# Optimization experiments

Measured on AMD Instinct MI355X. Metric: run time of the kernel, lower is better.

The kernel has to match this reference:

```python
import jax, jax.numpy as jnp
import numpy as np

D = 1024      # model_dimension
H = 16        # num_heads
HD = D // H   # head_dimension (shared K/V head dim)
B, S = 2, 2048


def setup_inputs() -> dict:
    key = jax.random.key(0)
    ks = jax.random.split(key, 11)
    s = 0.02
    return {
        "q": jax.random.normal(ks[0], (B, S, D), jnp.float32),
        "k": jax.random.normal(ks[1], (B, S, D), jnp.float32),
        "v": jax.random.normal(ks[2], (B, S, D), jnp.float32),
        "Wq": jax.random.normal(ks[3], (D, D), jnp.float32) * s,
        "bq": jnp.zeros((D,), jnp.float32),
        "Wk": jax.random.normal(ks[4], (D, HD), jnp.float32) * s,
        "bk": jnp.zeros((HD,), jnp.float32),
        "Wv": jax.random.normal(ks[5], (D, HD), jnp.float32) * s,
        "bv": jnp.zeros((HD,), jnp.float32),
        "Wo": jax.random.normal(ks[6], (D, D), jnp.float32) * s,
        "bo": jnp.zeros((D,), jnp.float32),
    }


def reference(q, k, v, Wq, bq, Wk, bk, Wv, bv, Wo, bo):
    Bsz, Sq, Dm = q.shape
    # Q projection + split into heads: (B, H, Sq, HD)
    qh = (q @ Wq + bq).reshape(Bsz, Sq, H, HD).transpose(0, 2, 1, 3)
    # Shared single K/V head: (B, Sk, HD)
    kh = k @ Wk + bk
    vh = v @ Wv + bv
    # Scores (B, H, Sq, Sk), scaled then clamped as in the original
    scores = jnp.einsum('bhqd,bkd->bhqk', qh, kh) / jnp.sqrt(jnp.float32(HD))
    scores = jnp.clip(scores, -1e6, 1e6)
    attn = jax.nn.softmax(scores, axis=-1)
    out = jnp.einsum('bhqk,bkd->bhqd', attn, vh)
    out = out.transpose(0, 2, 1, 3).reshape(Bsz, Sq, Dm)
    return out @ Wo + bo
```

## Files before the change

kernel.cpp:

```cpp
#include <hip/hip_runtime.h>
#include <cstdint>
#include <cstddef>

typedef unsigned short u16;
typedef uint32_t u32;
typedef __bf16 bf16x8 __attribute__((ext_vector_type(8)));
typedef float  f32x4  __attribute__((ext_vector_type(4)));
typedef u16    u16x4  __attribute__((ext_vector_type(4)));

#define DEV static __device__ __forceinline__
#define MFMA16(a, b, c) __builtin_amdgcn_mfma_f32_16x16x32_bf16(a, b, c, 0, 0, 0)

DEV u16 f2bf(float x) {
  unsigned u = __float_as_uint(x);
  u += 0x7fffu + ((u >> 16) & 1u);
  return (u16)(u >> 16);
}

DEV u32 cvt_pk_bf16(float lo, float hi) {
  u32 r;
  asm("v_cvt_pk_bf16_f32 %0, %1, %2" : "=v"(r) : "v"(lo), "v"(hi));
  return r;
}

DEV void gload_lds16(const void* g, void* l) {
  __builtin_amdgcn_global_load_lds(
      (__attribute__((address_space(1))) void*)(void*)g,
      (__attribute__((address_space(3))) void*)l, 16, 0, 0);
}

__global__ void k_convert3(const float* __restrict__ a, const float* __restrict__ b,
                           const float* __restrict__ c, u16* __restrict__ oa,
                           u16* __restrict__ ob, u16* __restrict__ oc, int n4) {
  int i = blockIdx.x * blockDim.x + threadIdx.x;
  if (i >= n4) return;
  const float* src = blockIdx.y == 0 ? a : blockIdx.y == 1 ? b : c;
  u16* dst = blockIdx.y == 0 ? oa : blockIdx.y == 1 ? ob : oc;
  f32x4 f = reinterpret_cast<const f32x4*>(src)[i];
  u16x4 o;
  o[0] = f2bf(f[0]); o[1] = f2bf(f[1]); o[2] = f2bf(f[2]); o[3] = f2bf(f[3]);
  reinterpret_cast<u16x4*>(dst)[i] = o;
}

__global__ void k_transpose2(const float* __restrict__ in0, u16* __restrict__ out0,
                             const float* __restrict__ in1, u16* __restrict__ out1,
                             int R, int C) {
  __shared__ float tile[32][33];
  const float* in = blockIdx.z ? in1 : in0;
  u16* out = blockIdx.z ? out1 : out0;
  int bx = blockIdx.x * 32, by = blockIdx.y * 32;
  int tx = threadIdx.x, ty = threadIdx.y;
#pragma unroll
  for (int j = 0; j < 4; ++j)
    tile[ty + j * 8][tx] = in[(size_t)(by + ty + j * 8) * C + bx + tx];
  __syncthreads();
#pragma unroll
  for (int j = 0; j < 4; ++j)
    out[(size_t)(bx + ty + j * 8) * R + by + tx] = f2bf(tile[tx][ty + j * 8]);
}

template <bool OUT_BF16>
__global__ __launch_bounds__(512) void k_gemm128(const u16* __restrict__ A, const u16* __restrict__ Bt,
                                                 const float* __restrict__ bias, void* __restrict__ Cout,
                                                 int M, int N, int K, float scale) {
  __shared__ u16 As[128 * 32];
  __shared__ u16 Bs[128 * 32];
  const int tid = threadIdx.x, lane = tid & 63, wid = tid >> 6;
  const int s = blockIdx.x;
  const int xr = s & 7, t = s >> 3;
  const int bx = t & 7;
  const int by = (t >> 3) * 8 + xr;
  const int brow = by * 128, bcol = bx * 128;
  const int wr = (wid >> 2) * 64, wc = (wid & 3) * 32;

  const int e0 = wid * 512 + lane * 8;
  const u16* a0 = A + (size_t)(brow + (e0 >> 5)) * K + (e0 & 31);
  const u16* b0 = Bt + (size_t)(bcol + (e0 >> 5)) * K + (e0 & 31);
  u16* lA = As + wid * 512;
  u16* lB = Bs + wid * 512;

  f32x4 acc[4][2] = {};
  for (int k0 = 0; k0 < K; k0 += 32) {
    gload_lds16(a0 + k0, lA);
    gload_lds16(b0 + k0, lB);
    __syncthreads();
    const int lr = lane & 15, lk = (lane >> 4) * 8;
    bf16x8 af[4], bfr[2];
#pragma unroll
    for (int m = 0; m < 4; ++m) af[m] = *(const bf16x8*)&As[(wr + m * 16 + lr) * 32 + lk];
#pragma unroll
    for (int n = 0; n < 2; ++n) bfr[n] = *(const bf16x8*)&Bs[(wc + n * 16 + lr) * 32 + lk];
#pragma unroll
    for (int m = 0; m < 4; ++m)
#pragma unroll
      for (int n = 0; n < 2; ++n) acc[m][n] = MFMA16(af[m], bfr[n], acc[m][n]);
    __syncthreads();
  }

  const int lr = lane & 15, lg = lane >> 4;
#pragma unroll
  for (int m = 0; m < 4; ++m)
#pragma unroll
    for (int n = 0; n < 2; ++n) {
      const int col = bcol + wc + n * 16 + lr;
      const float bv = bias ? bias[col] : 0.f;
#pragma unroll
      for (int r = 0; r < 4; ++r) {
        const int row = brow + wr + m * 16 + lg * 4 + r;
        float val = (acc[m][n][r] + bv) * scale;
        if constexpr (OUT_BF16) ((u16*)Cout)[(size_t)row * N + col] = f2bf(val);
        else ((float*)Cout)[(size_t)row * N + col] = val;
      }
    }
}

__global__ __launch_bounds__(256) void k_gemm64(const u16* __restrict__ A0, const u16* __restrict__ A1,
                                                const u16* __restrict__ Bt0, const u16* __restrict__ Bt1,
                                                const float* __restrict__ bias0, const float* __restrict__ bias1,
                                                u16* __restrict__ C0, u16* __restrict__ C1, int K) {
  __shared__ u16 As[64 * 32];
  __shared__ u16 Bs[64 * 32];
  const int sel = blockIdx.y;
  const u16* A = sel ? A1 : A0;
  const u16* Bt = sel ? Bt1 : Bt0;
  const float* bias = sel ? bias1 : bias0;
  const int tid = threadIdx.x, lane = tid & 63, wid = tid >> 6;
  const int brow = blockIdx.x * 64;
  const int e0 = wid * 512 + lane * 8;
  const u16* a0 = A + (size_t)(brow + (e0 >> 5)) * K + (e0 & 31);
  const u16* b0 = Bt + (size_t)(e0 >> 5) * K + (e0 & 31);
  u16* lA = As + wid * 512;
  u16* lB = Bs + wid * 512;
  f32x4 acc[4] = {};

  for (int k0 = 0; k0 < K; k0 += 32) {
    gload_lds16(a0 + k0, lA);
    gload_lds16(b0 + k0, lB);
    __syncthreads();
    const int lr = lane & 15, lk = (lane >> 4) * 8;
    bf16x8 af = *(const bf16x8*)&As[(wid * 16 + lr) * 32 + lk];
#pragma unroll
    for (int n = 0; n < 4; ++n) {
      bf16x8 bfr = *(const bf16x8*)&Bs[(n * 16 + lr) * 32 + lk];
      acc[n] = MFMA16(af, bfr, acc[n]);
    }
    __syncthreads();
  }

  const int lr = lane & 15, lg = lane >> 4;
#pragma unroll
  for (int n = 0; n < 4; ++n) {
    const int col = n * 16 + lr;
    const float bv = bias[col];
#pragma unroll
    for (int r = 0; r < 4; ++r) {
      const int row = brow + wid * 16 + lg * 4 + r;
      const float val = acc[n][r] + bv;
      if (sel)
        C1[((size_t)(row >> 11) * 64 + col) * 2048 + (row & 2047)] = f2bf(val);
      else
        C0[(size_t)row * 64 + col] = f2bf(val);
    }
  }
}

__global__ __launch_bounds__(512) void k_attn(const u16* __restrict__ Qh, const u16* __restrict__ Kh,
                                              const u16* __restrict__ VhT, u16* __restrict__ Out) {
  constexpr int S = 2048, D = 1024, NT = 32;
  __shared__ u16 Ks[2][64 * 64];
  __shared__ u16 Vs[2][64 * 64];
  __shared__ u16 Ps[8][16 * 64];
  const int lane = threadIdx.x & 63, wid = threadIdx.x >> 6;
  const int lr = lane & 15, lg = lane >> 4;
  const int q0 = blockIdx.x * 128;
  const int h = blockIdx.y, b = blockIdx.z;

  bf16x8 qf[2];
#pragma unroll
  for (int kk = 0; kk < 2; ++kk)
    qf[kk] = *(const bf16x8*)&Qh[(size_t)(b * S + q0 + wid * 16 + lr) * D + h * 64 + kk * 32 + lg * 8];

  const int r8 = lane >> 3, ssl = (lane & 7) ^ r8;
  const u16* ksrc = Kh + (size_t)(b * S + wid * 8 + r8) * 64 + ssl * 8;
  const u16* vsrc = VhT + (size_t)(b * 64 + wid * 8 + r8) * S + ssl * 8;

  float lsum = 0.f;
  f32x4 o[4] = {};
  u16* Pw = &Ps[wid][0];
  const int pswz = (lr & 7) << 3;

  auto STAGE = [&](int buf, int t) {
    gload_lds16(ksrc + (size_t)(t * 64) * 64, &Ks[buf][(wid * 8) * 64]);
    gload_lds16(vsrc + t * 64, &Vs[buf][(wid * 8) * 64]);
  };

  STAGE(0, 0);
#pragma unroll 1
  for (int t = 0; t < NT; ++t) {
    if (t + 1 < NT) {
      STAGE((t + 1) & 1, t + 1);
      asm volatile("s_waitcnt vmcnt(2)\n\ts_barrier" ::: "memory");
    } else {
      asm volatile("s_waitcnt vmcnt(0)\n\ts_barrier" ::: "memory");
    }
    __builtin_amdgcn_sched_barrier(0);

    const u16* Kb = &Ks[t & 1][0];
    const u16* Vb = &Vs[t & 1][0];

    f32x4 z[4] = {};
    __builtin_amdgcn_s_setprio(1);
#pragma unroll
    for (int kk = 0; kk < 2; ++kk)
#pragma unroll
      for (int ct = 0; ct < 4; ++ct) {
        const int row = ct * 16 + lr;
        bf16x8 kf = *(const bf16x8*)&Kb[row * 64 + (((kk * 4 + lg) ^ (row & 7)) << 3)];
        z[ct] = MFMA16(kf, qf[kk], z[ct]);
      }
    __builtin_amdgcn_s_setprio(0);

    float s = 0.f;
#pragma unroll
    for (int ct = 0; ct < 4; ++ct) {
      const float p0 = __builtin_amdgcn_exp2f(z[ct][0]);
      const float p1 = __builtin_amdgcn_exp2f(z[ct][1]);
      const float p2 = __builtin_amdgcn_exp2f(z[ct][2]);
      const float p3 = __builtin_amdgcn_exp2f(z[ct][3]);
      s += (p0 + p1) + (p2 + p3);
      uint2 pk;
      pk.x = cvt_pk_bf16(p0, p1);
      pk.y = cvt_pk_bf16(p2, p3);
      *(uint2*)&Pw[lr * 64 + ((ct * 16 + lg * 4) ^ pswz)] = pk;
    }
    lsum += s;

#pragma unroll
    for (int kk = 0; kk < 2; ++kk) {
      bf16x8 pa = *(const bf16x8*)&Pw[lr * 64 + ((kk * 32 + lg * 8) ^ pswz)];
      __builtin_amdgcn_s_setprio(1);
#pragma unroll
      for (int nt = 0; nt < 4; ++nt) {
        const int row = nt * 16 + lr;
        bf16x8 vf = *(const bf16x8*)&Vb[row * 64 + (((kk * 4 + lg) ^ (row & 7)) << 3)];
        o[nt] = MFMA16(pa, vf, o[nt]);
      }
      __builtin_amdgcn_s_setprio(0);
    }
    asm volatile("s_barrier" ::: "memory");
  }

  lsum += __shfl_xor(lsum, 16);
  lsum += __shfl_xor(lsum, 32);
  const float linv = 1.f / lsum;
#pragma unroll
  for (int r = 0; r < 4; ++r) {
    const float li = __shfl(linv, (lane & 48) | (lg * 4 + r));
    const size_t row = (size_t)(b * S + q0 + wid * 16 + lg * 4 + r);
#pragma unroll
    for (int nt = 0; nt < 4; ++nt)
      Out[row * D + h * 64 + nt * 16 + lr] = f2bf(o[nt][r] * li);
  }
}

extern "C" void kernel_launch(void* const* d_in, const int* in_sizes, int n_in,
                              void* d_out, int out_size, void* d_ws, size_t ws_size,
                              hipStream_t stream) {
  const float* q  = (const float*)d_in[0];
  const float* k  = (const float*)d_in[1];
  const float* v  = (const float*)d_in[2];
  const float* Wq = (const float*)d_in[3];
  const float* bq = (const float*)d_in[4];
  const float* Wk = (const float*)d_in[5];
  const float* bk = (const float*)d_in[6];
  const float* Wv = (const float*)d_in[7];
  const float* bv = (const float*)d_in[8];
  const float* Wo = (const float*)d_in[9];
  const float* bo = (const float*)d_in[10];
  float* out = (float*)d_out;

  constexpr int B = 2, S = 2048, D = 1024, H = 16, HDc = 64;
  constexpr int M = B * S;

  char* ws = (char*)d_ws;
  size_t off = 0;
  auto alloc = [&](size_t bytes) { char* p = ws + off; off += bytes; return p; };
  u16* q_bf = (u16*)alloc((size_t)M * D * 2);
  u16* k_bf = (u16*)alloc((size_t)M * D * 2);
  u16* v_bf = (u16*)alloc((size_t)M * D * 2);
  u16* WqT  = (u16*)alloc((size_t)D * D * 2);
  u16* WkvT = (u16*)alloc((size_t)2 * HDc * D * 2);
  u16* WoT  = (u16*)alloc((size_t)D * D * 2);
  u16* Qh   = (u16*)alloc((size_t)M * D * 2);
  u16* Kh   = (u16*)alloc((size_t)M * HDc * 2);
  u16* VhT  = (u16*)alloc((size_t)M * HDc * 2);
  u16* WkT = WkvT;
  u16* WvT = WkvT + (size_t)HDc * D;
  u16* AO = q_bf;

  {
    int n4 = M * D / 4;
    k_convert3<<<dim3((n4 + 255) / 256, 3), 256, 0, stream>>>(q, k, v, q_bf, k_bf, v_bf, n4);
  }
  k_transpose2<<<dim3(D / 32, D / 32, 2), dim3(32, 8), 0, stream>>>(Wq, WqT, Wo, WoT, D, D);
  k_transpose2<<<dim3(HDc / 32, D / 32, 2), dim3(32, 8), 0, stream>>>(Wk, WkT, Wv, WvT, D, HDc);
  k_gemm128<true><<<dim3((M / 128) * (D / 128)), 512, 0, stream>>>(q_bf, WqT, bq, Qh, M, D, D,
                                                                   0.125f * 1.44269504089f);
  k_gemm64<<<dim3(M / 64, 2), 256, 0, stream>>>(k_bf, v_bf, WkT, WvT, bk, bv, Kh, VhT, D);
  k_attn<<<dim3(S / 128, H, B), 512, 0, stream>>>(Qh, Kh, VhT, AO);
  k_gemm128<false><<<dim3((M / 128) * (D / 128)), 512, 0, stream>>>(AO, WoT, bo, out, M, D, D, 1.0f);
}
```

Measured before the change: 128.2 us.

## Double-buffer LDS tiles in GEMM to overlap global loads with MFMA

```diff
diff --git a/kernel.cpp b/kernel.cpp
--- a/kernel.cpp
+++ b/kernel.cpp
@@ -63,8 +63,8 @@
 __global__ __launch_bounds__(512) void k_gemm128(const u16* __restrict__ A, const u16* __restrict__ Bt,
                                                  const float* __restrict__ bias, void* __restrict__ Cout,
                                                  int M, int N, int K, float scale) {
-  __shared__ u16 As[128 * 32];
-  __shared__ u16 Bs[128 * 32];
+  __shared__ u16 As[2][128 * 32];
+  __shared__ u16 Bs[2][128 * 32];
   const int tid = threadIdx.x, lane = tid & 63, wid = tid >> 6;
   const int s = blockIdx.x;
   const int xr = s & 7, t = s >> 3;
@@ -76,25 +76,40 @@
   const int e0 = wid * 512 + lane * 8;
   const u16* a0 = A + (size_t)(brow + (e0 >> 5)) * K + (e0 & 31);
   const u16* b0 = Bt + (size_t)(bcol + (e0 >> 5)) * K + (e0 & 31);
-  u16* lA = As + wid * 512;
-  u16* lB = Bs + wid * 512;
+
+  auto STAGE = [&](int buf, int k0) {
+    gload_lds16(a0 + k0, &As[buf][wid * 512]);
+    gload_lds16(b0 + k0, &Bs[buf][wid * 512]);
+  };
 
   f32x4 acc[4][2] = {};
-  for (int k0 = 0; k0 < K; k0 += 32) {
-    gload_lds16(a0 + k0, lA);
-    gload_lds16(b0 + k0, lB);
-    __syncthreads();
+  const int NK = K / 32;
+  STAGE(0, 0);
+#pragma unroll 1
+  for (int ks = 0; ks < NK; ++ks) {
+    if (ks + 1 < NK) {
+      STAGE((ks + 1) & 1, (ks + 1) * 32);
+      asm volatile("s_waitcnt vmcnt(2)\n\ts_barrier" ::: "memory");
+    } else {
+      asm volatile("s_waitcnt vmcnt(0)\n\ts_barrier" ::: "memory");
+    }
+    __builtin_amdgcn_sched_barrier(0);
+
+    const u16* Ab = &As[ks & 1][0];
+    const u16* Bb = &Bs[ks & 1][0];
     const int lr = lane & 15, lk = (lane >> 4) * 8;
     bf16x8 af[4], bfr[2];
 #pragma unroll
-    for (int m = 0; m < 4; ++m) af[m] = *(const bf16x8*)&As[(wr + m * 16 + lr) * 32 + lk];
-#pragma unroll
-    for (int n = 0; n < 2; ++n) bfr[n] = *(const bf16x8*)&Bs[(wc + n * 16 + lr) * 32 + lk];
+    for (int m = 0; m < 4; ++m) af[m] = *(const bf16x8*)&Ab[(wr + m * 16 + lr) * 32 + lk];
+#pragma unroll
+    for (int n = 0; n < 2; ++n) bfr[n] = *(const bf16x8*)&Bb[(wc + n * 16 + lr) * 32 + lk];
+    __builtin_amdgcn_s_setprio(1);
 #pragma unroll
     for (int m = 0; m < 4; ++m)
 #pragma unroll
       for (int n = 0; n < 2; ++n) acc[m][n] = MFMA16(af[m], bfr[n], acc[m][n]);
-    __syncthreads();
+    __builtin_amdgcn_s_setprio(0);
+    asm volatile("s_barrier" ::: "memory");
   }
 
   const int lr = lane & 15, lg = lane >> 4;
```

After: 125.4 us. 2.2% less time.
